# Optimization experiments

Measured on AMD Instinct MI355X. Metric: run time of the kernel, lower is better.

The kernel has to match this reference:

```python
import jax, jax.numpy as jnp
import numpy as np

D = 2048
H = 16
DH = D // H
L = 512  # kv_latent_dim
LN_EPS = 1e-5


def setup_inputs() -> dict:
    key = jax.random.key(0)
    ks = jax.random.split(key, 8)
    s = 0.02  # weight init scale to keep logits in a sane range
    x = jax.random.normal(ks[0], (2, 2048, D), dtype=jnp.float32)
    W_q = jax.random.normal(ks[1], (D, D), dtype=jnp.float32) * s      # torch Linear weight [out,in]
    Wd_kv = jax.random.normal(ks[2], (L, D), dtype=jnp.float32) * s
    W_uv = jax.random.normal(ks[3], (D, L), dtype=jnp.float32) * s
    W_uk = jax.random.normal(ks[4], (D, L), dtype=jnp.float32) * s
    W_o = jax.random.normal(ks[5], (D, D), dtype=jnp.float32) * s
    gamma = jnp.ones((L,), dtype=jnp.float32)
    beta = jnp.zeros((L,), dtype=jnp.float32)
    return {"x": x, "W_q": W_q, "Wd_kv": Wd_kv, "W_uv": W_uv, "W_uk": W_uk,
            "W_o": W_o, "gamma": gamma, "beta": beta}


def _layernorm(h, gamma, beta):
    mu = jnp.mean(h, axis=-1, keepdims=True)
    var = jnp.mean(jnp.square(h - mu), axis=-1, keepdims=True)
    return (h - mu) * jax.lax.rsqrt(var + LN_EPS) * gamma + beta


def reference(x, W_q, Wd_kv, W_uv, W_uk, W_o, gamma, beta):
    B, S, _ = x.shape
    # absorbed K projection: (W_q @ W_uk) -> [H, dh, L]
    absorbed_k = (W_q @ W_uk).reshape(H, DH, L)
    # latent KV: layernorm(x @ Wd_kv^T), [B, S, L]
    c_kv = _layernorm(jnp.einsum('bsd,ld->bsl', x, Wd_kv), gamma, beta)
    S_full = c_kv.shape[1]
    # NOTE: original uses raw x (not W_q(x)) as q; W_q is folded into absorbed_k
    q = x.reshape(B, S, H, DH)
    tmp = jnp.einsum('bshd,hdl->bhsl', q, absorbed_k)              # [B,H,S,L]
    scores = jnp.einsum('bhsl,btl->bhst', tmp, c_kv) / np.sqrt(DH)  # [B,H,S,S_full]
    # causal mask (past_length=0)
    mask = jnp.tril(jnp.ones((S, S_full), dtype=bool), k=0)
    scores = jnp.where(mask[None, None], scores, -jnp.inf)
    attn = jax.nn.softmax(scores, axis=-1)
    v_full = jnp.einsum('btl,dl->btd', c_kv, W_uv).reshape(B, S_full, H, DH)
    ctx = jnp.einsum('bhst,bthd->bshd', attn, v_full).reshape(B, S, D)
    out = jnp.einsum('bsd,od->bso', ctx, W_o)
    return out, c_kv
```

## Files before the change

kernel.cpp:

```cpp
#include <hip/hip_runtime.h>
#include <hip/hip_bf16.h>
#include <cstdint>


typedef __bf16 bf16x8 __attribute__((ext_vector_type(8)));
typedef __bf16 bf16x4 __attribute__((ext_vector_type(4)));
typedef float  f32x4  __attribute__((ext_vector_type(4)));

#define GLOBAL_AS __attribute__((address_space(1)))
#define LDS_AS    __attribute__((address_space(3)))

__device__ __forceinline__ void gload_lds16(const void* g, void* l) {
    __builtin_amdgcn_global_load_lds((const GLOBAL_AS uint32_t*)g,
                                     (LDS_AS uint32_t*)l, 16, 0, 0);
}

__global__ void k_cast_all(const float* __restrict__ x, const float* __restrict__ wq,
                           const float* __restrict__ wdkv, const float* __restrict__ wuv,
                           const float* __restrict__ wo,
                           __bf16* __restrict__ xb, __bf16* __restrict__ wqb,
                           __bf16* __restrict__ wdkvb, __bf16* __restrict__ wuvb,
                           __bf16* __restrict__ wob) {
    long i = (long)blockIdx.x * blockDim.x + threadIdx.x;
    const float* src; __bf16* dst; long off;
    if (i < 1048576)      { src = x;    dst = xb;    off = i; }
    else if (i < 1572864) { src = wq;   dst = wqb;   off = i - 1048576; }
    else if (i < 1703936) { src = wdkv; dst = wdkvb; off = i - 1572864; }
    else if (i < 1835008) { src = wuv;  dst = wuvb;  off = i - 1703936; }
    else                  { src = wo;   dst = wob;   off = i - 1835008; }
    long e = off * 8;
    float4 a = *reinterpret_cast<const float4*>(src + e);
    float4 b = *reinterpret_cast<const float4*>(src + e + 4);
    bf16x8 r;
    r[0] = (__bf16)a.x; r[1] = (__bf16)a.y; r[2] = (__bf16)a.z; r[3] = (__bf16)a.w;
    r[4] = (__bf16)b.x; r[5] = (__bf16)b.y; r[6] = (__bf16)b.z; r[7] = (__bf16)b.w;
    *reinterpret_cast<bf16x8*>(dst + e) = r;
}

__global__ void k_transpose_wuk(const float* __restrict__ in, __bf16* __restrict__ out) {
    __shared__ float t[64][65];
    const int d0 = blockIdx.x * 64, l0 = blockIdx.y * 64;
    const int tid = threadIdx.x;
    const int r = tid >> 4, c = (tid & 15) * 4;
    #pragma unroll
    for (int rr = 0; rr < 64; rr += 16) {
        float4 v = *reinterpret_cast<const float4*>(&in[(long)(d0 + r + rr) * 512 + l0 + c]);
        t[r + rr][c] = v.x; t[r + rr][c + 1] = v.y;
        t[r + rr][c + 2] = v.z; t[r + rr][c + 3] = v.w;
    }
    __syncthreads();
    const int lr = tid >> 2, dc = (tid & 3) * 16;
    bf16x8 o0, o1;
    #pragma unroll
    for (int i = 0; i < 8; ++i) { o0[i] = (__bf16)t[dc + i][lr]; o1[i] = (__bf16)t[dc + 8 + i][lr]; }
    *reinterpret_cast<bf16x8*>(&out[(long)(l0 + lr) * 2048 + d0 + dc]) = o0;
    *reinterpret_cast<bf16x8*>(&out[(long)(l0 + lr) * 2048 + d0 + dc + 8]) = o1;
}

template <typename CT, int WR>
__global__ __launch_bounds__(256, 2) void k_gemm_bt(
    const __bf16* __restrict__ A, const __bf16* __restrict__ B, CT* __restrict__ C,
    int K, int lda, int ldb, int ldc,
    long aOffZ, long bOffZ, long cOffZ, float cmul)
{
    constexpr int WC   = 4 / WR;
    constexpr int BN   = WC * 64;
    constexpr int WRB  = 128 / WR;
    constexpr int MREP = WRB / 16;
    constexpr int BCH  = BN / 32;
    A += (long)blockIdx.z * aOffZ;
    B += (long)blockIdx.z * bOffZ;
    C += (long)blockIdx.z * cOffZ;
    __shared__ __bf16 Asm[128][64];
    __shared__ __bf16 Bsm[BN][64];
    const int tid  = threadIdx.x;
    const int lane = tid & 63, wid = tid >> 6;
    const int wr = wid / WC, wc = wid % WC;
    const int tm = blockIdx.x * 128, tn = blockIdx.y * BN;
    const int r16 = lane & 15, g = lane >> 4;

    const int srow  = lane >> 3;
    const int sslot = lane & 7;
    const int scol  = ((sslot ^ srow) * 8);

    f32x4 acc[MREP][4];
    #pragma unroll
    for (int m = 0; m < MREP; ++m)
        #pragma unroll
        for (int n = 0; n < 4; ++n) acc[m][n] = (f32x4){0.f, 0.f, 0.f, 0.f};

    for (int kt = 0; kt < K; kt += 64) {
        __syncthreads();
        #pragma unroll
        for (int c2 = 0; c2 < 4; ++c2) {
            const int chunk = wid * 4 + c2;
            const int row   = chunk * 8 + srow;
            gload_lds16(&A[(long)(tm + row) * lda + kt + scol], &Asm[chunk * 8][0]);
        }
        #pragma unroll
        for (int c2 = 0; c2 < BCH; ++c2) {
            const int chunk = wid * BCH + c2;
            const int row   = chunk * 8 + srow;
            gload_lds16(&B[(long)(tn + row) * ldb + kt + scol], &Bsm[chunk * 8][0]);
        }
        __syncthreads();
        #pragma unroll
        for (int kk = 0; kk < 2; ++kk) {
            bf16x8 af[MREP], bfr[4];
            #pragma unroll
            for (int m = 0; m < MREP; ++m) {
                const int row = wr * WRB + m * 16 + r16;
                af[m] = *reinterpret_cast<const bf16x8*>(
                    reinterpret_cast<const char*>(&Asm[0][0]) +
                    row * 128 + (((kk * 4 + g) ^ (row & 7)) * 16));
            }
            #pragma unroll
            for (int n = 0; n < 4; ++n) {
                const int row = wc * 64 + n * 16 + r16;
                bfr[n] = *reinterpret_cast<const bf16x8*>(
                    reinterpret_cast<const char*>(&Bsm[0][0]) +
                    row * 128 + (((kk * 4 + g) ^ (row & 7)) * 16));
            }
            #pragma unroll
            for (int m = 0; m < MREP; ++m)
                #pragma unroll
                for (int n = 0; n < 4; ++n)
                    acc[m][n] = __builtin_amdgcn_mfma_f32_16x16x32_bf16(af[m], bfr[n], acc[m][n], 0, 0, 0);
        }
    }
    #pragma unroll
    for (int m = 0; m < MREP; ++m) {
        #pragma unroll
        for (int n = 0; n < 4; ++n) {
            #pragma unroll
            for (int j = 0; j < 4; ++j) {
                const int row = tm + wr * WRB + m * 16 + g * 4 + j;
                const int col = tn + wc * 64 + n * 16 + r16;
                C[(long)row * ldc + col] = (CT)(acc[m][n][j] * cmul);
            }
        }
    }
}

__global__ void k_layernorm(const float* __restrict__ pre, const float* __restrict__ gamma,
                            const float* __restrict__ beta, float* __restrict__ out_f32,
                            __bf16* __restrict__ out_bf16) {
    const int row  = blockIdx.x * 4 + (threadIdx.x >> 6);
    const int lane = threadIdx.x & 63;
    const float* p = pre + (long)row * 512;
    float4 v0 = *reinterpret_cast<const float4*>(p + lane * 4);
    float4 v1 = *reinterpret_cast<const float4*>(p + 256 + lane * 4);
    float s  = v0.x + v0.y + v0.z + v0.w + v1.x + v1.y + v1.z + v1.w;
    float s2 = v0.x*v0.x + v0.y*v0.y + v0.z*v0.z + v0.w*v0.w
             + v1.x*v1.x + v1.y*v1.y + v1.z*v1.z + v1.w*v1.w;
    #pragma unroll
    for (int d = 1; d < 64; d <<= 1) { s += __shfl_xor(s, d); s2 += __shfl_xor(s2, d); }
    const float mu  = s * (1.0f / 512.0f);
    const float var = s2 * (1.0f / 512.0f) - mu * mu;
    const float rs  = rsqrtf(var + 1e-5f);
    float4 g0 = *reinterpret_cast<const float4*>(gamma + lane * 4);
    float4 g1 = *reinterpret_cast<const float4*>(gamma + 256 + lane * 4);
    float4 b0 = *reinterpret_cast<const float4*>(beta + lane * 4);
    float4 b1 = *reinterpret_cast<const float4*>(beta + 256 + lane * 4);
    float4 y0, y1;
    y0.x = (v0.x - mu) * rs * g0.x + b0.x;  y0.y = (v0.y - mu) * rs * g0.y + b0.y;
    y0.z = (v0.z - mu) * rs * g0.z + b0.z;  y0.w = (v0.w - mu) * rs * g0.w + b0.w;
    y1.x = (v1.x - mu) * rs * g1.x + b1.x;  y1.y = (v1.y - mu) * rs * g1.y + b1.y;
    y1.z = (v1.z - mu) * rs * g1.z + b1.z;  y1.w = (v1.w - mu) * rs * g1.w + b1.w;
    *reinterpret_cast<float4*>(out_f32 + (long)row * 512 + lane * 4) = y0;
    *reinterpret_cast<float4*>(out_f32 + (long)row * 512 + 256 + lane * 4) = y1;
    bf16x4 z0, z1;
    z0[0] = (__bf16)y0.x; z0[1] = (__bf16)y0.y; z0[2] = (__bf16)y0.z; z0[3] = (__bf16)y0.w;
    z1[0] = (__bf16)y1.x; z1[1] = (__bf16)y1.y; z1[2] = (__bf16)y1.z; z1[3] = (__bf16)y1.w;
    *reinterpret_cast<bf16x4*>(out_bf16 + (long)row * 512 + lane * 4) = z0;
    *reinterpret_cast<bf16x4*>(out_bf16 + (long)row * 512 + 256 + lane * 4) = z1;
}

__global__ __launch_bounds__(256, 2) void k_attn(
    const __bf16* __restrict__ xb,
    const __bf16* __restrict__ Keff,
    const __bf16* __restrict__ vT,
    __bf16* __restrict__ ctx)
{
    __shared__ __bf16 Ks[2][64][128];
    __shared__ __bf16 Vs[2][128][64];
    __shared__ __bf16 Pl[4][16][72];
    const int lane = threadIdx.x & 63;
    const int wid  = threadIdx.x >> 6;
    const int r16  = lane & 15;
    const int g    = lane >> 4;
    const int bid  = blockIdx.x;
    const int gidx = ((bid >> 7) << 3) | (bid & 7);
    const int h = gidx & 15, b = gidx >> 4;
    const int p = (bid >> 3) & 15;
    const int nkt = 32 - p;
    const int qbase[2] = { p * 64 + wid * 16, (31 - p) * 64 + wid * 16 };

    bf16x8 aQ[2][4];
    #pragma unroll
    for (int st = 0; st < 2; ++st) {
        const __bf16* qp = xb + ((long)(b * 2048 + qbase[st] + r16)) * 2048 + h * 128 + g * 8;
        #pragma unroll
        for (int ks = 0; ks < 4; ++ks)
            aQ[st][ks] = *reinterpret_cast<const bf16x8*>(qp + ks * 32);
    }

    f32x4 o[2][8];
    float mrow[2], lrow[2];
    #pragma unroll
    for (int st = 0; st < 2; ++st) {
        #pragma unroll
        for (int d8 = 0; d8 < 8; ++d8) o[st][d8] = (f32x4){0.f, 0.f, 0.f, 0.f};
        mrow[st] = -__builtin_inff(); lrow[st] = 0.f;
    }

    const __bf16* Kb = Keff + (long)h * (4096 * 128) + (long)b * (2048 * 128);
    const __bf16* Vb = vT + (long)h * (128 * 4096) + b * 2048;

    const int ksrow = wid * 4 + (lane >> 4);
    const int kslot = lane & 15;
    const int vsrow = wid * 8 + (lane >> 3);
    const int vslot = lane & 7;

    auto stage = [&](int kt, int buf) {
        const int k0s = kt * 64;
        #pragma unroll
        for (int c = 0; c < 4; ++c) {
            const int row = c * 16 + ksrow;
            const int gcol = ((kslot ^ (row & 15)) << 3);
            gload_lds16(&Kb[(long)(k0s + row) * 128 + gcol], &Ks[buf][c * 16 + wid * 4][0]);
        }
        #pragma unroll
        for (int c = 0; c < 4; ++c) {
            const int row = c * 32 + vsrow;
            const int gcol = ((vslot ^ (row & 7)) << 3);
            gload_lds16(&Vb[(long)row * 4096 + k0s + gcol], &Vs[buf][c * 32 + wid * 8][0]);
        }
    };

    const float THR = 11.541560327f;
    stage(0, 0);
    for (int kt = 0; kt < nkt; ++kt) {
        const int cur = kt & 1;
        const int k0 = kt * 64;
        __syncthreads();
        if (kt + 1 < nkt) stage(kt + 1, cur ^ 1);
        const char* Kbase = reinterpret_cast<const char*>(&Ks[cur][0][0]);
        const char* Vbase = reinterpret_cast<const char*>(&Vs[cur][0][0]);
        const bool light = (kt <= p);

        f32x4 sT[2][4];
        #pragma unroll
        for (int kh = 0; kh < 4; ++kh) {
            sT[0][kh] = (f32x4){0.f, 0.f, 0.f, 0.f};
            sT[1][kh] = (f32x4){0.f, 0.f, 0.f, 0.f};
        }
        __builtin_amdgcn_s_setprio(1);
        #pragma unroll
        for (int kh = 0; kh < 4; ++kh) {
            const int krow = kh * 16 + r16;
            bf16x8 bk[4];
            #pragma unroll
            for (int ks = 0; ks < 4; ++ks)
                bk[ks] = *reinterpret_cast<const bf16x8*>(
                    Kbase + krow * 256 + (((ks * 4 + g) ^ (krow & 15)) * 16));
            #pragma unroll
            for (int ks = 0; ks < 4; ++ks)
                sT[1][kh] = __builtin_amdgcn_mfma_f32_16x16x32_bf16(bk[ks], aQ[1][ks], sT[1][kh], 0, 0, 0);
            if (light) {
                #pragma unroll
                for (int ks = 0; ks < 4; ++ks)
                    sT[0][kh] = __builtin_amdgcn_mfma_f32_16x16x32_bf16(bk[ks], aQ[0][ks], sT[0][kh], 0, 0, 0);
            }
        }
        __builtin_amdgcn_s_setprio(0);

        bf16x8 pa[2][2];
        #pragma unroll
        for (int sti = 0; sti < 2; ++sti) {
            const int st = 1 - sti;
            if (st == 0 && !light) continue;
            const bool diag = (st == 0) ? (kt == p) : (kt == nkt - 1);
            float sc[16];
            #pragma unroll
            for (int kh = 0; kh < 4; ++kh)
                #pragma unroll
                for (int j = 0; j < 4; ++j) sc[kh * 4 + j] = sT[st][kh][j];
            if (diag) {
                const int qabs = qbase[st] + r16;
                #pragma unroll
                for (int kh = 0; kh < 4; ++kh)
                    #pragma unroll
                    for (int j = 0; j < 4; ++j)
                        if (k0 + kh * 16 + g * 4 + j > qabs) sc[kh * 4 + j] = -1e30f;
            }
            float t01 = fmaxf(sc[0], sc[1]),  t23 = fmaxf(sc[2], sc[3]);
            float t45 = fmaxf(sc[4], sc[5]),  t67 = fmaxf(sc[6], sc[7]);
            float t89 = fmaxf(sc[8], sc[9]),  tab = fmaxf(sc[10], sc[11]);
            float tcd = fmaxf(sc[12], sc[13]), tef = fmaxf(sc[14], sc[15]);
            float tmax = fmaxf(fmaxf(fmaxf(t01, t23), fmaxf(t45, t67)),
                               fmaxf(fmaxf(t89, tab), fmaxf(tcd, tef)));
            tmax = fmaxf(tmax, __shfl_xor(tmax, 16));
            tmax = fmaxf(tmax, __shfl_xor(tmax, 32));
            const int needi = !__all(tmax <= mrow[st] + THR);
            float m = mrow[st], alpha = 1.f;
            if (needi) {
                const float mnew = fmaxf(m, tmax);
                alpha = __builtin_amdgcn_exp2f(m - mnew);
                m = mnew; mrow[st] = mnew;
            }
            float rsum = 0.f;
            bf16x4 pb[4];
            #pragma unroll
            for (int kh = 0; kh < 4; ++kh) {
                #pragma unroll
                for (int j = 0; j < 4; ++j) {
                    const float pv = __builtin_amdgcn_exp2f(sc[kh * 4 + j] - m);
                    rsum += pv;
                    pb[kh][j] = (__bf16)pv;
                }
            }
            rsum += __shfl_xor(rsum, 16);
            rsum += __shfl_xor(rsum, 32);
            lrow[st] = lrow[st] * alpha + rsum;
            #pragma unroll
            for (int kh = 0; kh < 4; ++kh)
                *reinterpret_cast<bf16x4*>(&Pl[wid][r16][kh * 16 + g * 4]) = pb[kh];
            pa[st][0] = *reinterpret_cast<const bf16x8*>(&Pl[wid][r16][g * 8]);
            pa[st][1] = *reinterpret_cast<const bf16x8*>(&Pl[wid][r16][32 + g * 8]);
            if (needi) {
                float a4[4];
                #pragma unroll
                for (int j = 0; j < 4; ++j) a4[j] = __shfl(alpha, g * 4 + j);
                #pragma unroll
                for (int d8 = 0; d8 < 8; ++d8) {
                    o[st][d8][0] *= a4[0]; o[st][d8][1] *= a4[1];
                    o[st][d8][2] *= a4[2]; o[st][d8][3] *= a4[3];
                }
            }
        }

        __builtin_amdgcn_s_setprio(1);
        #pragma unroll
        for (int kk = 0; kk < 2; ++kk) {
            #pragma unroll
            for (int d8 = 0; d8 < 8; ++d8) {
                const int vrow = d8 * 16 + r16;
                bf16x8 bv = *reinterpret_cast<const bf16x8*>(
                    Vbase + vrow * 128 + (((kk * 4 + g) ^ (vrow & 7)) * 16));
                o[1][d8] = __builtin_amdgcn_mfma_f32_16x16x32_bf16(pa[1][kk], bv, o[1][d8], 0, 0, 0);
                if (light)
                    o[0][d8] = __builtin_amdgcn_mfma_f32_16x16x32_bf16(pa[0][kk], bv, o[0][d8], 0, 0, 0);
            }
        }
        __builtin_amdgcn_s_setprio(0);
    }
    #pragma unroll
    for (int st = 0; st < 2; ++st) {
        float rl4[4];
        #pragma unroll
        for (int j = 0; j < 4; ++j) rl4[j] = 1.0f / __shfl(lrow[st], g * 4 + j);
        #pragma unroll
        for (int d8 = 0; d8 < 8; ++d8) {
            #pragma unroll
            for (int j = 0; j < 4; ++j) {
                const int row = qbase[st] + g * 4 + j;
                ctx[((long)(b * 2048 + row)) * 2048 + h * 128 + d8 * 16 + r16] =
                    (__bf16)(o[st][d8][j] * rl4[j]);
            }
        }
    }
}

extern "C" void kernel_launch(void* const* d_in, const int* in_sizes, int n_in,
                              void* d_out, int out_size, void* d_ws, size_t ws_size,
                              hipStream_t stream) {
    const float* x     = (const float*)d_in[0];
    const float* W_q   = (const float*)d_in[1];
    const float* Wd_kv = (const float*)d_in[2];
    const float* W_uv  = (const float*)d_in[3];
    const float* W_uk  = (const float*)d_in[4];
    const float* W_o   = (const float*)d_in[5];
    const float* gamma = (const float*)d_in[6];
    const float* beta  = (const float*)d_in[7];
    float* out     = (float*)d_out;
    float* ckv_out = out + 8388608;

    char* ws = (char*)d_ws;
    __bf16* xb     = (__bf16*)(ws + 0);
    __bf16* Wqb    = (__bf16*)(ws + 16777216);
    __bf16* Wdkvb  = (__bf16*)(ws + 25165824);
    __bf16* Wuvb   = (__bf16*)(ws + 27262976);
    __bf16* Wob    = (__bf16*)(ws + 29360128);
    __bf16* WukT   = (__bf16*)(ws + 37748736);
    __bf16* absk   = (__bf16*)(ws + 39845888);
    float*  ckvpre = (float*) (ws + 41943040);
    __bf16* ckvb   = (__bf16*)(ws + 50331648);
    __bf16* Keff   = (__bf16*)(ws + 54525952);
    __bf16* vT     = (__bf16*)(ws + 71303168);
    __bf16* ctx    = (__bf16*)(ws + 88080384);

    k_cast_all<<<9216, 256, 0, stream>>>(x, W_q, Wd_kv, W_uv, W_o,
                                         xb, Wqb, Wdkvb, Wuvb, Wob);
    k_transpose_wuk<<<dim3(32, 8), 256, 0, stream>>>(W_uk, WukT);

    const float cscale = 1.4426950408889634f * 0.08838834764831845f;
    k_gemm_bt<__bf16, 4><<<dim3(16, 8, 1), 256, 0, stream>>>(Wqb, WukT, absk,
        2048, 2048, 2048, 512, 0, 0, 0, cscale);
    k_gemm_bt<float, 4><<<dim3(32, 8, 1), 256, 0, stream>>>(xb, Wdkvb, ckvpre,
        2048, 2048, 2048, 512, 0, 0, 0, 1.0f);
    k_layernorm<<<1024, 256, 0, stream>>>(ckvpre, gamma, beta, ckv_out, ckvb);
    k_gemm_bt<__bf16, 2><<<dim3(32, 1, 16), 256, 0, stream>>>(ckvb, absk, Keff,
        512, 512, 512, 128, 0, 128 * 512, 4096 * 128, 1.0f);
    k_gemm_bt<__bf16, 2><<<dim3(16, 32, 1), 256, 0, stream>>>(Wuvb, ckvb, vT,
        512, 512, 512, 4096, 0, 0, 0, 1.0f);
    k_attn<<<512, 256, 0, stream>>>(xb, Keff, vT, ctx);
    k_gemm_bt<float, 2><<<dim3(32, 16, 1), 256, 0, stream>>>(ctx, Wob, out,
        2048, 2048, 2048, 2048, 0, 0, 0, 1.0f);
}
```

Baseline: 215.8 us.

## Load V fragments directly from global memory instead of staging through LDS

Drops the LDS double buffer for V in the attention kernel. Each wave now reads its V fragments straight from global memory into registers, issuing the first half before the softmax and the second half between the two PV MFMA groups. This halves shared memory use, so launch bounds are raised to allow three blocks per CU. In exchange, all four waves redundantly read V tiles from global/L2 without async staging, and holding the extra registers under the tighter occupancy target may cause spills.

```diff
diff --git a/kernel.cpp b/kernel.cpp
--- a/kernel.cpp
+++ b/kernel.cpp
@@ -176,14 +176,13 @@
     *reinterpret_cast<bf16x4*>(out_bf16 + (long)row * 512 + 256 + lane * 4) = z1;
 }
 
-__global__ __launch_bounds__(256, 2) void k_attn(
+__global__ __launch_bounds__(256, 3) void k_attn(
     const __bf16* __restrict__ xb,
     const __bf16* __restrict__ Keff,
     const __bf16* __restrict__ vT,
     __bf16* __restrict__ ctx)
 {
     __shared__ __bf16 Ks[2][64][128];
-    __shared__ __bf16 Vs[2][128][64];
     __shared__ __bf16 Pl[4][16][72];
     const int lane = threadIdx.x & 63;
     const int wid  = threadIdx.x >> 6;
@@ -219,8 +218,6 @@
 
     const int ksrow = wid * 4 + (lane >> 4);
     const int kslot = lane & 15;
-    const int vsrow = wid * 8 + (lane >> 3);
-    const int vslot = lane & 7;
 
     auto stage = [&](int kt, int buf) {
         const int k0s = kt * 64;
@@ -229,12 +226,6 @@
             const int row = c * 16 + ksrow;
             const int gcol = ((kslot ^ (row & 15)) << 3);
             gload_lds16(&Kb[(long)(k0s + row) * 128 + gcol], &Ks[buf][c * 16 + wid * 4][0]);
-        }
-        #pragma unroll
-        for (int c = 0; c < 4; ++c) {
-            const int row = c * 32 + vsrow;
-            const int gcol = ((vslot ^ (row & 7)) << 3);
-            gload_lds16(&Vb[(long)row * 4096 + k0s + gcol], &Vs[buf][c * 32 + wid * 8][0]);
         }
     };
 
@@ -246,7 +237,6 @@
         __syncthreads();
         if (kt + 1 < nkt) stage(kt + 1, cur ^ 1);
         const char* Kbase = reinterpret_cast<const char*>(&Ks[cur][0][0]);
-        const char* Vbase = reinterpret_cast<const char*>(&Vs[cur][0][0]);
         const bool light = (kt <= p);
 
         f32x4 sT[2][4];
@@ -274,6 +264,12 @@
             }
         }
         __builtin_amdgcn_s_setprio(0);
+
+        bf16x8 bv0[8];
+        #pragma unroll
+        for (int d8 = 0; d8 < 8; ++d8)
+            bv0[d8] = *reinterpret_cast<const bf16x8*>(
+                Vb + (long)(d8 * 16 + r16) * 4096 + k0 + g * 8);
 
         bf16x8 pa[2][2];
         #pragma unroll
@@ -281,23 +277,18 @@
             const int st = 1 - sti;
             if (st == 0 && !light) continue;
             const bool diag = (st == 0) ? (kt == p) : (kt == nkt - 1);
-            float sc[16];
-            #pragma unroll
-            for (int kh = 0; kh < 4; ++kh)
-                #pragma unroll
-                for (int j = 0; j < 4; ++j) sc[kh * 4 + j] = sT[st][kh][j];
             if (diag) {
                 const int qabs = qbase[st] + r16;
                 #pragma unroll
                 for (int kh = 0; kh < 4; ++kh)
                     #pragma unroll
                     for (int j = 0; j < 4; ++j)
-                        if (k0 + kh * 16 + g * 4 + j > qabs) sc[kh * 4 + j] = -1e30f;
-            }
-            float t01 = fmaxf(sc[0], sc[1]),  t23 = fmaxf(sc[2], sc[3]);
-            float t45 = fmaxf(sc[4], sc[5]),  t67 = fmaxf(sc[6], sc[7]);
-            float t89 = fmaxf(sc[8], sc[9]),  tab = fmaxf(sc[10], sc[11]);
-            float tcd = fmaxf(sc[12], sc[13]), tef = fmaxf(sc[14], sc[15]);
+                        if (k0 + kh * 16 + g * 4 + j > qabs) sT[st][kh][j] = -1e30f;
+            }
+            float t01 = fmaxf(sT[st][0][0], sT[st][0][1]), t23 = fmaxf(sT[st][0][2], sT[st][0][3]);
+            float t45 = fmaxf(sT[st][1][0], sT[st][1][1]), t67 = fmaxf(sT[st][1][2], sT[st][1][3]);
+            float t89 = fmaxf(sT[st][2][0], sT[st][2][1]), tab = fmaxf(sT[st][2][2], sT[st][2][3]);
+            float tcd = fmaxf(sT[st][3][0], sT[st][3][1]), tef = fmaxf(sT[st][3][2], sT[st][3][3]);
             float tmax = fmaxf(fmaxf(fmaxf(t01, t23), fmaxf(t45, t67)),
                                fmaxf(fmaxf(t89, tab), fmaxf(tcd, tef)));
             tmax = fmaxf(tmax, __shfl_xor(tmax, 16));
@@ -315,7 +306,7 @@
             for (int kh = 0; kh < 4; ++kh) {
                 #pragma unroll
                 for (int j = 0; j < 4; ++j) {
-                    const float pv = __builtin_amdgcn_exp2f(sc[kh * 4 + j] - m);
+                    const float pv = __builtin_amdgcn_exp2f(sT[st][kh][j] - m);
                     rsum += pv;
                     pb[kh][j] = (__bf16)pv;
                 }
@@ -342,16 +333,23 @@
 
         __builtin_amdgcn_s_setprio(1);
         #pragma unroll
-        for (int kk = 0; kk < 2; ++kk) {
-            #pragma unroll
-            for (int d8 = 0; d8 < 8; ++d8) {
-                const int vrow = d8 * 16 + r16;
-                bf16x8 bv = *reinterpret_cast<const bf16x8*>(
-                    Vbase + vrow * 128 + (((kk * 4 + g) ^ (vrow & 7)) * 16));
-                o[1][d8] = __builtin_amdgcn_mfma_f32_16x16x32_bf16(pa[1][kk], bv, o[1][d8], 0, 0, 0);
-                if (light)
-                    o[0][d8] = __builtin_amdgcn_mfma_f32_16x16x32_bf16(pa[0][kk], bv, o[0][d8], 0, 0, 0);
-            }
+        for (int d8 = 0; d8 < 8; ++d8) {
+            o[1][d8] = __builtin_amdgcn_mfma_f32_16x16x32_bf16(pa[1][0], bv0[d8], o[1][d8], 0, 0, 0);
+            if (light)
+                o[0][d8] = __builtin_amdgcn_mfma_f32_16x16x32_bf16(pa[0][0], bv0[d8], o[0][d8], 0, 0, 0);
+        }
+        __builtin_amdgcn_s_setprio(0);
+        bf16x8 bv1[8];
+        #pragma unroll
+        for (int d8 = 0; d8 < 8; ++d8)
+            bv1[d8] = *reinterpret_cast<const bf16x8*>(
+                Vb + (long)(d8 * 16 + r16) * 4096 + k0 + 32 + g * 8);
+        __builtin_amdgcn_s_setprio(1);
+        #pragma unroll
+        for (int d8 = 0; d8 < 8; ++d8) {
+            o[1][d8] = __builtin_amdgcn_mfma_f32_16x16x32_bf16(pa[1][1], bv1[d8], o[1][d8], 0, 0, 0);
+            if (light)
+                o[0][d8] = __builtin_amdgcn_mfma_f32_16x16x32_bf16(pa[0][1], bv1[d8], o[0][d8], 0, 0, 0);
         }
         __builtin_amdgcn_s_setprio(0);
     }
```

Result: slower. 357.8 us (+65.8%).
